# Optimization experiments

Measured on AMD Instinct MI355X. Metric: run time of the kernel, lower is better.

Reference implementation:

```python
import jax, jax.numpy as jnp
import numpy as np
from jax import lax

B, IC, OC, H, W_DIM, K = 8, 64, 64, 256, 512, 3
BLUR_1D = [1.0, 3.0, 3.0, 1.0]
FACTOR = 2
GAIN = 1.0


def _blur_kernel():
    # setup_resample_kernel: outer product of 1D kernel, normalized to sum 1
    k = np.asarray(BLUR_1D, dtype=np.float32)
    k = np.outer(k, k)
    k = k / np.sum(k)
    return k  # [4,4]


def setup_inputs() -> dict:
    key = jax.random.key(0)
    ks = jax.random.split(key, 5)
    x = jax.random.normal(ks[0], (B, IC, H, H), dtype=jnp.float32)
    w = jax.random.normal(ks[1], (B, W_DIM), dtype=jnp.float32)
    # init_std = 1.0 for both weights since lrmul = 1.0
    w_conv = jax.random.normal(ks[2], (K, K, IC, OC), dtype=jnp.float32)
    w_dense = jax.random.normal(ks[3], (W_DIM, IC), dtype=jnp.float32)
    b_mod = jnp.zeros((IC,), dtype=jnp.float32)
    return {"x": x, "w": w, "w_conv": w_conv, "w_dense": w_dense, "b_mod": b_mod}


def reference(x, w, w_conv, w_dense, b_mod):
    k = w_conv.shape[0]
    ic, oc = w_conv.shape[2], w_conv.shape[3]

    # runtime coefs (equalized lr): he_std = gain / sqrt(fan_in), lrmul = 1
    coef_conv = 1.0 / np.sqrt(k * k * ic)
    coef_dense = 1.0 / np.sqrt(w.shape[1])

    # style = Dense(w) + bias (linear act, gain 1) + 1.0   -> [B, IC]
    style = w @ (coef_dense * w_dense) + b_mod + 1.0

    # modulate: [B,k,k,IC,OC]
    wmod = (coef_conv * w_conv)[None] * style[:, None, None, :, None]
    # demodulate over (kh, kw, ic)
    d = lax.rsqrt(jnp.sum(jnp.square(wmod), axis=(1, 2, 3)) + 1e-8)  # [B,OC]
    wmod = wmod * d[:, None, None, None, :]

    # per-sample grouped transposed conv (upsample x2) == lhs-dilated cross-corr
    # with the unflipped modulated weight, padding k-1 on each side.
    w_oihw = jnp.transpose(wmod, (0, 4, 3, 1, 2))  # [B,OC,IC,k,k]

    def up_conv(xb, wb):
        return lax.conv_general_dilated(
            xb[None], wb, window_strides=(1, 1),
            padding=[(k - 1, k - 1), (k - 1, k - 1)],
            lhs_dilation=(FACTOR, FACTOR),
            dimension_numbers=("NCHW", "OIHW", "NCHW"))[0]

    y = jax.vmap(up_conv)(x, w_oihw)  # [B,OC,(H-1)*2+k,(W-1)*2+k] = [B,OC,513,513]

    # upfirdn blur: kernel scaled by gain * factor**2, pad0 = pad1 = 1,
    # true convolution (kernel flipped in reference) applied depthwise.
    kb = jnp.asarray(_blur_kernel() * (GAIN * FACTOR ** 2))  # [4,4]
    fw = kb[::-1, ::-1][None, None]  # [1,1,4,4]
    b_, c_, s1, s2 = y.shape
    y = lax.conv_general_dilated(
        y.reshape(b_ * c_, 1, s1, s2), fw, window_strides=(1, 1),
        padding=[(1, 1), (1, 1)],
        dimension_numbers=("NCHW", "OIHW", "NCHW"))
    # output spatial: s1 + 2 - 4 + 1 = 2H
    return y.reshape(b_, c_, y.shape[2], y.shape[3])
```

## Files before the change

kernel.cpp:

```cpp
#include <hip/hip_runtime.h>

#define NB 8
#define IC 64
#define OC 64
#define HH 256
#define WD 512
#define PP 258

typedef __bf16 bf16x8 __attribute__((ext_vector_type(8)));
typedef float f32x16 __attribute__((ext_vector_type(16)));
typedef float f32x2 __attribute__((ext_vector_type(2)));
typedef unsigned int u32;

__device__ inline void compute_E(const float* __restrict__ w_conv, float stv,
                                 int oc, float E[6][6]) {
  const float coef_conv = 1.0f / 24.0f;
  const float s = stv * coef_conv;
  const int ic = threadIdx.x & 63;

  float wm[3][3];
  float ssq = 0.f;
  #pragma unroll
  for (int kh = 0; kh < 3; ++kh)
    #pragma unroll
    for (int kw = 0; kw < 3; ++kw) {
      float v = w_conv[((kh * 3 + kw) * IC + ic) * OC + oc] * s;
      wm[kh][kw] = v;
      ssq += v * v;
    }
  #pragma unroll
  for (int off = 32; off > 0; off >>= 1) ssq += __shfl_xor(ssq, off);
  const float d = rsqrtf(ssq + 1e-8f);
  #pragma unroll
  for (int kh = 0; kh < 3; ++kh)
    #pragma unroll
    for (int kw = 0; kw < 3; ++kw) wm[kh][kw] *= d;

  const float g[4] = {0.25f, 0.75f, 0.75f, 0.25f};
  #pragma unroll
  for (int a = 0; a < 6; ++a)
    #pragma unroll
    for (int c = 0; c < 6; ++c) {
      float acc = 0.f;
      #pragma unroll
      for (int dh = 0; dh < 3; ++dh) {
        int u = a - dh;
        if (u < 0 || u > 3) continue;
        #pragma unroll
        for (int dw = 0; dw < 3; ++dw) {
          int v = c - dw;
          if (v < 0 || v > 3) continue;
          acc = fmaf(wm[dh][dw], g[u] * g[v], acc);
        }
      }
      E[a][c] = acc;
    }
}

__device__ inline float style_of(const float* __restrict__ w,
                                 const float* __restrict__ w_dense,
                                 const float* __restrict__ b_mod, int b,
                                 int ic) {
  const float coef_dense = 0.044194173824159216f;
  const float* wr = w + b * WD;
  float acc = 0.f;
  for (int k = 0; k < WD; ++k) acc = fmaf(wr[k], w_dense[k * IC + ic], acc);
  return acc * coef_dense + b_mod[ic] + 1.0f;
}

__global__ __launch_bounds__(64) void pwfs_kernel(
    const float* __restrict__ w, const float* __restrict__ w_dense,
    const float* __restrict__ b_mod, const float* __restrict__ w_conv,
    __bf16* __restrict__ PWf) {
  const int oc = blockIdx.x;
  const int b = blockIdx.y;
  const int ic = threadIdx.x;

  float stv = style_of(w, w_dense, b_mod, b, ic);
  float E[6][6];
  compute_E(w_conv, stv, oc, E);

  const int ks = ic >> 4;
  const int h = (ic >> 3) & 1;
  const int e = ic & 7;
  const int lane = (oc & 31) + 32 * h;
  const int ocg = oc >> 5;

  #pragma unroll
  for (int pp = 0; pp < 2; ++pp)
    #pragma unroll
    for (int pq = 0; pq < 2; ++pq) {
      const int ph = pp * 2 + pq;
      #pragma unroll
      for (int j = 0; j < 3; ++j)
        #pragma unroll
        for (int l = 0; l < 3; ++l) {
          const int tap = j * 3 + l;
          float val = E[2 * j + 1 - pp][2 * l + 1 - pq];
          size_t off =
              ((size_t)(((((b * 4 + ph) * 9 + tap) * 2 + ocg) * 4 + ks)) * 64 +
               lane) * 8 + e;
          PWf[off] = (__bf16)val;
        }
    }
}

__global__ __launch_bounds__(256) void xtp_kernel(const float* __restrict__ x,
                                                  __bf16* __restrict__ xTg) {
  __shared__ unsigned short buf[64 * 260];
  const int tid = threadIdx.x;
  const int m = blockIdx.x;
  const int b = blockIdx.y;

  if (m == 256) {
    uint4 z = make_uint4(0, 0, 0, 0);
    for (int i = tid; i < 8224; i += 256) {
      int pix = i >> 3;
      int sub = i & 7;
      int pr, pc;
      if (pix < 258) {
        pr = 0; pc = pix;
      } else if (pix < 516) {
        pr = 257; pc = pix - 258;
      } else {
        int rem = pix - 516;
        pr = 1 + (rem >> 1);
        pc = (rem & 1) ? 257 : 0;
      }
      *(uint4*)(xTg + ((size_t)(b * PP + pr) * PP + pc) * 64 + sub * 8) = z;
    }
    return;
  }

  const int ln = tid & 63, grp = tid >> 6;
  #pragma unroll
  for (int p = 0; p < 16; ++p) {
    const int ic = p * 4 + grp;
    float4 v = *(const float4*)(x + ((size_t)(b * 64 + ic) * 256 + m) * 256 +
                                ln * 4);
    ushort4 u4;
    u4.x = __builtin_bit_cast(unsigned short, (__bf16)v.x);
    u4.y = __builtin_bit_cast(unsigned short, (__bf16)v.y);
    u4.z = __builtin_bit_cast(unsigned short, (__bf16)v.z);
    u4.w = __builtin_bit_cast(unsigned short, (__bf16)v.w);
    *(ushort4*)&buf[ic * 260 + ln * 4] = u4;
  }
  __syncthreads();
  #pragma unroll
  for (int it = 0; it < 8; ++it) {
    int pix = it * 32 + (tid >> 3);
    int g = tid & 7;
    bf16x8 o;
    #pragma unroll
    for (int e = 0; e < 8; ++e)
      o[e] = __builtin_bit_cast(__bf16, buf[(g * 8 + e) * 260 + pix]);
    *(bf16x8*)(xTg + ((size_t)(b * PP + m + 1) * PP + (pix + 1)) * 64 +
               g * 8) = o;
  }
}

#define CMT 16
#define CNT 32
#define XR 18
#define XC 34

__device__ __forceinline__ void loadA(const bf16x8* __restrict__ Av, int phb,
                                      int ocg, int ks, int l, int lane,
                                      bf16x8 A[3][2]) {
  #pragma unroll
  for (int j = 0; j < 3; ++j) {
    const int tap = j * 3 + l;
    #pragma unroll
    for (int pq = 0; pq < 2; ++pq)
      A[j][pq] =
          Av[(size_t)((((phb + pq) * 9 + tap) * 2 + ocg) * 4 + ks) * 64 + lane];
  }
}

#define GLD_LDS(src, dst)                                                \
  __builtin_amdgcn_global_load_lds(                                      \
      (const __attribute__((address_space(1))) void*)(src),              \
      (__attribute__((address_space(3))) void*)(dst), 16, 0, 0)

__device__ __forceinline__ void stage_tile(const __bf16* __restrict__ xTg,
                                           int b, int m0, int n0,
                                           __bf16* xsbuf, int wv, int lane) {
  const int r0 = (18 * wv) >> 3;
  const int r1 = (18 * (wv + 1)) >> 3;
  for (int row = r0; row < r1; ++row) {
    const size_t srow = (size_t)(b * PP + m0 + row) * PP;
    __bf16* ldsrow = xsbuf + row * (XC * 64);
    #pragma unroll
    for (int q = 0; q < 4; ++q) {
      int pix = q * 8 + (lane >> 3);
      int g = (lane & 7) ^ (pix & 7);
      const __bf16* src = xTg + (srow + (n0 + pix)) * 64 + g * 8;
      GLD_LDS(src, ldsrow + q * 512);
    }
    if (lane < 16) {
      int pix = 32 + (lane >> 3);
      int g = (lane & 7) ^ (pix & 7);
      const __bf16* src = xTg + (srow + (n0 + pix)) * 64 + g * 8;
      GLD_LDS(src, ldsrow + 2048);
    }
  }
}

__global__ __launch_bounds__(512, 2) void conv32p_kernel(
    const __bf16* __restrict__ xTg, const __bf16* __restrict__ PWf,
    float* __restrict__ out) {
  __shared__ __bf16 xs[2][XR * XC * 64];

  const int tid = threadIdx.x;
  const int lane = tid & 63;
  const int wv = tid >> 6;
  const int pp = wv & 1;
  const int rh = wv >> 1;

  const int bid = blockIdx.x;
  const int ngrp = bid & 1;
  const int mtile = (bid >> 1) & 15;
  const int ocg = (bid >> 5) & 1;
  const int b = bid >> 6;
  const int m0 = mtile * CMT;

  const int ln31 = lane & 31;
  const int lh = lane >> 5;
  const bf16x8* Av = (const bf16x8*)PWf;
  const int phb = b * 4 + pp * 2;

  stage_tile(xTg, b, m0, ngrp * 128, &xs[0][0], wv, lane);
  asm volatile("s_waitcnt vmcnt(0)" ::: "memory");
  __builtin_amdgcn_s_barrier();

  #pragma unroll 1
  for (int t = 0; t < 4; ++t) {
    const int n0 = ngrp * 128 + t * 32;
    if (t < 3)
      stage_tile(xTg, b, m0, n0 + 32, &xs[(t + 1) & 1][0], wv, lane);

    const __bf16* xb = &xs[t & 1][0];

    f32x16 acc[4][2];
    #pragma unroll
    for (int mw = 0; mw < 4; ++mw)
      #pragma unroll
      for (int pq = 0; pq < 2; ++pq)
        #pragma unroll
        for (int e = 0; e < 16; ++e) acc[mw][pq][e] = 0.f;

    bf16x8 Ac[3][2], An[3][2];
    loadA(Av, phb, ocg, 0, 0, lane, Ac);

    int ks = 0, l = 0;
    #pragma unroll 1
    for (int it = 0; it < 12; ++it) {
      const int ln = (l == 2) ? 0 : l + 1;
      const int ksn = ((l == 2) ? ks + 1 : ks) & 3;
      loadA(Av, phb, ocg, ksn, ln, lane, An);

      bf16x8 Bf[6];
      const int col_t = ln31 + l;
      const int gneed = ks * 2 + lh;
      #pragma unroll
      for (int r = 0; r < 6; ++r) {
        const int lds_row = 4 * rh + r;
        Bf[r] = *(const bf16x8*)(xb + ((lds_row * XC + col_t) * 8 +
                                       (gneed ^ (col_t & 7))) * 8);
      }

      __builtin_amdgcn_s_setprio(1);
      #pragma unroll
      for (int r = 0; r < 6; ++r) {
        #pragma unroll
        for (int j = 0; j < 3; ++j) {
          const int mw = r - j;
          if (mw >= 0 && mw < 4) {
            acc[mw][0] = __builtin_amdgcn_mfma_f32_32x32x16_bf16(
                Ac[j][0], Bf[r], acc[mw][0], 0, 0, 0);
            acc[mw][1] = __builtin_amdgcn_mfma_f32_32x32x16_bf16(
                Ac[j][1], Bf[r], acc[mw][1], 0, 0, 0);
          }
        }
      }
      __builtin_amdgcn_s_setprio(0);

      #pragma unroll
      for (int j = 0; j < 3; ++j)
        #pragma unroll
        for (int pq = 0; pq < 2; ++pq) Ac[j][pq] = An[j][pq];
      ks = ksn;
      l = ln;
    }

    #pragma unroll
    for (int mw = 0; mw < 4; ++mw) {
      const int p = 2 * (m0 + 4 * rh + mw) + pp;
      #pragma unroll
      for (int rr = 0; rr < 16; ++rr) {
        const int oc_loc = (rr & 3) + 8 * (rr >> 2) + 4 * lh;
        const int oc = ocg * 32 + oc_loc;
        size_t off =
            ((size_t)(b * 64 + oc) * 512 + p) * 512 + 2 * n0 + 2 * ln31;
        f32x2 v2;
        v2[0] = acc[mw][0][rr];
        v2[1] = acc[mw][1][rr];
        *(f32x2*)(out + off) = v2;
      }
    }

    asm volatile("s_waitcnt vmcnt(63)" ::: "memory");
    __builtin_amdgcn_s_barrier();
  }
}

__global__ __launch_bounds__(256) void xt_kernel(const float* __restrict__ x,
                                                 __bf16* __restrict__ xT) {
  __shared__ unsigned short buf[64 * 257];
  const int tid = threadIdx.x;
  const int m = blockIdx.x;
  const int b = blockIdx.y;

  for (int ic = 0; ic < 64; ++ic) {
    float v = x[((size_t)(b * 64 + ic) * 256 + m) * 256 + tid];
    buf[ic * 257 + tid] = __builtin_bit_cast(unsigned short, (__bf16)v);
  }
  __syncthreads();
  bf16x8* xTv = (bf16x8*)xT;
  #pragma unroll
  for (int it = 0; it < 8; ++it) {
    int pix = it * 32 + (tid >> 3);
    int g = tid & 7;
    bf16x8 o;
    #pragma unroll
    for (int e = 0; e < 8; ++e)
      o[e] = __builtin_bit_cast(__bf16, buf[(g * 8 + e) * 257 + pix]);
    xTv[((size_t)(b * 256 + m) * 256 + pix) * 8 + g] = o;
  }
}

__global__ __launch_bounds__(512, 2) void conv32_kernel(
    const __bf16* __restrict__ xT, const __bf16* __restrict__ PWf,
    float* __restrict__ out) {
  __shared__ bf16x8 xs[XR * XC * 8];

  const int tid = threadIdx.x;
  const int lane = tid & 63;
  const int w = tid >> 6;
  const int pp = w & 1;
  const int rh = w >> 1;

  const int bx = blockIdx.x;
  const int mtile = bx >> 3;
  const int ntile = bx & 7;
  const int ocg = blockIdx.y;
  const int b = blockIdx.z;
  const int m0 = mtile * CMT;
  const int n0 = ntile * CNT;

  const bf16x8* xTv = (const bf16x8*)xT;
  #pragma unroll
  for (int itr = 0; itr < 10; ++itr) {
    int lin = itr * 512 + tid;
    if (lin < XR * XC * 8) {
      int g = lin & 7;
      int pix = lin >> 3;
      int col = pix % XC;
      int row = pix / XC;
      int gr = m0 - 1 + row;
      int gc = n0 - 1 + col;
      bf16x8 v;
      if ((unsigned)gr < 256u && (unsigned)gc < 256u) {
        v = xTv[((size_t)(b * 256 + gr) * 256 + gc) * 8 + g];
      } else {
        #pragma unroll
        for (int e = 0; e < 8; ++e) v[e] = (__bf16)0.f;
      }
      xs[pix * 8 + (g ^ (col & 7))] = v;
    }
  }
  __syncthreads();

  f32x16 acc[4][2];
  #pragma unroll
  for (int mw = 0; mw < 4; ++mw)
    #pragma unroll
    for (int pq = 0; pq < 2; ++pq)
      #pragma unroll
      for (int e = 0; e < 16; ++e) acc[mw][pq][e] = 0.f;

  const int ln31 = lane & 31;
  const int lh = lane >> 5;
  const bf16x8* Av = (const bf16x8*)PWf;
  const int phb = b * 4 + pp * 2;

  bf16x8 Ac[3][2], An[3][2];
  loadA(Av, phb, ocg, 0, 0, lane, Ac);

  int ks = 0, l = 0;
  #pragma unroll 1
  for (int it = 0; it < 12; ++it) {
    const int ln = (l == 2) ? 0 : l + 1;
    const int ksn = ((l == 2) ? ks + 1 : ks) & 3;
    loadA(Av, phb, ocg, ksn, ln, lane, An);

    bf16x8 Bf[6];
    const int col_t = ln31 + l;
    const int gneed = ks * 2 + lh;
    #pragma unroll
    for (int r = 0; r < 6; ++r) {
      const int lds_row = 4 * rh + r;
      Bf[r] = xs[(lds_row * XC + col_t) * 8 + (gneed ^ (col_t & 7))];
    }

    __builtin_amdgcn_s_setprio(1);
    #pragma unroll
    for (int r = 0; r < 6; ++r) {
      #pragma unroll
      for (int j = 0; j < 3; ++j) {
        const int mw = r - j;
        if (mw >= 0 && mw < 4) {
          acc[mw][0] = __builtin_amdgcn_mfma_f32_32x32x16_bf16(
              Ac[j][0], Bf[r], acc[mw][0], 0, 0, 0);
          acc[mw][1] = __builtin_amdgcn_mfma_f32_32x32x16_bf16(
              Ac[j][1], Bf[r], acc[mw][1], 0, 0, 0);
        }
      }
    }
    __builtin_amdgcn_s_setprio(0);

    #pragma unroll
    for (int j = 0; j < 3; ++j)
      #pragma unroll
      for (int pq = 0; pq < 2; ++pq) Ac[j][pq] = An[j][pq];
    ks = ksn;
    l = ln;
  }

  #pragma unroll
  for (int mw = 0; mw < 4; ++mw) {
    const int p = 2 * (m0 + 4 * rh + mw) + pp;
    #pragma unroll
    for (int rr = 0; rr < 16; ++rr) {
      const int oc_loc = (rr & 3) + 8 * (rr >> 2) + 4 * lh;
      const int oc = ocg * 32 + oc_loc;
      size_t off = ((size_t)(b * 64 + oc) * 512 + p) * 512 + 2 * n0 + 2 * ln31;
      f32x2 v2;
      v2[0] = acc[mw][0][rr];
      v2[1] = acc[mw][1][rr];
      *(f32x2*)(out + off) = v2;
    }
  }
}

__global__ __launch_bounds__(64) void pw_kernel(
    const float* __restrict__ w, const float* __restrict__ w_dense,
    const float* __restrict__ b_mod, const float* __restrict__ w_conv,
    float* __restrict__ PW) {
  const int oc = blockIdx.x;
  const int b = blockIdx.y;
  const int ic = threadIdx.x;
  float stv = style_of(w, w_dense, b_mod, b, ic);
  float E[6][6];
  compute_E(w_conv, stv, oc, E);
  #pragma unroll
  for (int pp = 0; pp < 2; ++pp)
    #pragma unroll
    for (int pq = 0; pq < 2; ++pq)
      #pragma unroll
      for (int j = 0; j < 3; ++j)
        #pragma unroll
        for (int l = 0; l < 3; ++l)
          PW[(((size_t)((b * 4 + pp * 2 + pq) * OC + oc) * IC + ic) * 9) +
             j * 3 + l] = E[2 * j + 1 - pp][2 * l + 1 - pq];
}

#define MT 16
#define NT 64
#define ICC 8
#define XROWS 18
#define XCOLS 66
#define XSTRIDE 68

__global__ __launch_bounds__(256) void conv_kernel(
    const float* __restrict__ x, const float* __restrict__ PW,
    float* __restrict__ out) {
  __shared__ float lds_x[ICC][XROWS][XSTRIDE];
  __shared__ float lds_w[4][ICC][9][4];

  const int tid = threadIdx.x;
  const int tn = tid & 15;
  const int tm = tid >> 4;
  const int bx = blockIdx.x;
  const int ntile = bx & 3;
  const int mtile = bx >> 2;
  const int ocg = blockIdx.y;
  const int b = blockIdx.z;
  const int m0 = mtile * MT;
  const int n0 = ntile * NT;

  float acc[4][4][4];
  #pragma unroll
  for (int o = 0; o < 4; ++o)
    #pragma unroll
    for (int ph = 0; ph < 4; ++ph)
      #pragma unroll
      for (int s = 0; s < 4; ++s) acc[o][ph][s] = 0.f;

  for (int ic0 = 0; ic0 < IC; ic0 += ICC) {
    __syncthreads();
    for (int ici = 0; ici < ICC; ++ici) {
      const float* xsrc = x + (size_t)(b * IC + ic0 + ici) * HH * HH;
      for (int rc = tid; rc < XROWS * XCOLS; rc += 256) {
        int r = rc / XCOLS;
        int c = rc - r * XCOLS;
        int gr = m0 - 1 + r;
        int gc = n0 - 1 + c;
        float v = 0.f;
        if ((unsigned)gr < HH && (unsigned)gc < HH) v = xsrc[gr * HH + gc];
        lds_x[ici][r][c] = v;
      }
    }
    for (int idx = tid; idx < 4 * ICC * 9 * 4; idx += 256) {
      int o = idx / (ICC * 9 * 4);
      int rem = idx - o * (ICC * 9 * 4);
      int ici = rem / 36;
      int r2 = rem - ici * 36;
      int t = r2 >> 2;
      int ph = r2 & 3;
      lds_w[o][ici][t][ph] =
          PW[(((size_t)((b * 4 + ph) * OC + (ocg * 4 + o)) * IC +
               (ic0 + ici)) * 9) + t];
    }
    __syncthreads();
    for (int ici = 0; ici < ICC; ++ici) {
      #pragma unroll
      for (int j = 0; j < 3; ++j) {
        const float* xr = &lds_x[ici][tm + j][tn * 4];
        float4 a4 = *(const float4*)xr;
        float2 a2 = *(const float2*)(xr + 4);
        float xv[6] = {a4.x, a4.y, a4.z, a4.w, a2.x, a2.y};
        #pragma unroll
        for (int l = 0; l < 3; ++l) {
          #pragma unroll
          for (int o = 0; o < 4; ++o) {
            float4 wv = *(const float4*)&lds_w[o][ici][j * 3 + l][0];
            #pragma unroll
            for (int s = 0; s < 4; ++s) {
              acc[o][0][s] = fmaf(wv.x, xv[l + s], acc[o][0][s]);
              acc[o][1][s] = fmaf(wv.y, xv[l + s], acc[o][1][s]);
              acc[o][2][s] = fmaf(wv.z, xv[l + s], acc[o][2][s]);
              acc[o][3][s] = fmaf(wv.w, xv[l + s], acc[o][3][s]);
            }
          }
        }
      }
    }
  }

  #pragma unroll
  for (int o = 0; o < 4; ++o) {
    #pragma unroll
    for (int pp = 0; pp < 2; ++pp) {
      const int p = 2 * (m0 + tm) + pp;
      float* dst = out +
          (((size_t)(b * OC + ocg * 4 + o) * 512 + p) * 512) + 2 * n0 + 8 * tn;
      float4 v0 = make_float4(acc[o][pp * 2 + 0][0], acc[o][pp * 2 + 1][0],
                              acc[o][pp * 2 + 0][1], acc[o][pp * 2 + 1][1]);
      float4 v1 = make_float4(acc[o][pp * 2 + 0][2], acc[o][pp * 2 + 1][2],
                              acc[o][pp * 2 + 0][3], acc[o][pp * 2 + 1][3]);
      *(float4*)dst = v0;
      *(float4*)(dst + 4) = v1;
    }
  }
}

extern "C" void kernel_launch(void* const* d_in, const int* in_sizes, int n_in,
                              void* d_out, int out_size, void* d_ws,
                              size_t ws_size, hipStream_t stream) {
  const float* x = (const float*)d_in[0];
  const float* w = (const float*)d_in[1];
  const float* w_conv = (const float*)d_in[2];
  const float* w_dense = (const float*)d_in[3];
  const float* b_mod = (const float*)d_in[4];
  float* out = (float*)d_out;

  const size_t PWF_BYTES = (size_t)8 * 4 * 9 * 2 * 4 * 64 * 8 * 2;
  const size_t XTG_BYTES = (size_t)8 * PP * PP * 64 * 2;
  const size_t XT_BYTES = (size_t)8 * 256 * 256 * 64 * 2;
  const size_t NEED_NEW = PWF_BYTES + XTG_BYTES;
  const size_t NEED_OLD = PWF_BYTES + XT_BYTES;

  if (ws_size >= NEED_NEW) {
    __bf16* PWf = (__bf16*)d_ws;
    __bf16* xTg = (__bf16*)((char*)d_ws + PWF_BYTES);
    pwfs_kernel<<<dim3(OC, NB), 64, 0, stream>>>(w, w_dense, b_mod, w_conv,
                                                 PWf);
    xtp_kernel<<<dim3(257, NB), 256, 0, stream>>>(x, xTg);
    conv32p_kernel<<<dim3(512), 512, 0, stream>>>(xTg, PWf, out);
  } else if (ws_size >= NEED_OLD) {
    __bf16* PWf = (__bf16*)d_ws;
    __bf16* xT = (__bf16*)((char*)d_ws + PWF_BYTES);
    pwfs_kernel<<<dim3(OC, NB), 64, 0, stream>>>(w, w_dense, b_mod, w_conv,
                                                 PWf);
    xt_kernel<<<dim3(256, NB), 256, 0, stream>>>(x, xT);
    conv32_kernel<<<dim3(128, 2, NB), 512, 0, stream>>>(xT, PWf, out);
  } else {
    float* PW = (float*)d_ws;
    pw_kernel<<<dim3(OC, NB), 64, 0, stream>>>(w, w_dense, b_mod, w_conv, PW);
    conv_kernel<<<dim3(64, 16, NB), 256, 0, stream>>>(x, PW, out);
  }
}
```

Measured before the change: 285.1 us.

## Split conv tile across 16 waves, drop A prefetch, add nontemporal stores

The main conv kernel now runs with 1024 threads per block. Each wave computes 2 output rows instead of 4, using fewer accumulators and B fragments, and the register double-buffering of A weight fragments is removed. Output stores become nontemporal, and the transpose kernel's LDS row stride is widened to change bank mapping. The unused fallback path and its kernels are removed. The intent is higher wave-level parallelism and less register pressure, at the cost of more redundant A loads and LDS reads per output, and no overlap of A loads with MFMA work.

```diff
diff --git a/kernel.cpp b/kernel.cpp
--- a/kernel.cpp
+++ b/kernel.cpp
@@ -10,7 +10,6 @@
 typedef __bf16 bf16x8 __attribute__((ext_vector_type(8)));
 typedef float f32x16 __attribute__((ext_vector_type(16)));
 typedef float f32x2 __attribute__((ext_vector_type(2)));
-typedef unsigned int u32;
 
 __device__ inline void compute_E(const float* __restrict__ w_conv, float stv,
                                  int oc, float E[6][6]) {
@@ -105,9 +104,10 @@
     }
 }
 
+#define XS 268
 __global__ __launch_bounds__(256) void xtp_kernel(const float* __restrict__ x,
                                                   __bf16* __restrict__ xTg) {
-  __shared__ unsigned short buf[64 * 260];
+  __shared__ unsigned short buf[64 * XS];
   const int tid = threadIdx.x;
   const int m = blockIdx.x;
   const int b = blockIdx.y;
@@ -143,7 +143,7 @@
     u4.y = __builtin_bit_cast(unsigned short, (__bf16)v.y);
     u4.z = __builtin_bit_cast(unsigned short, (__bf16)v.z);
     u4.w = __builtin_bit_cast(unsigned short, (__bf16)v.w);
-    *(ushort4*)&buf[ic * 260 + ln * 4] = u4;
+    *(ushort4*)&buf[ic * XS + ln * 4] = u4;
   }
   __syncthreads();
   #pragma unroll
@@ -153,7 +153,7 @@
     bf16x8 o;
     #pragma unroll
     for (int e = 0; e < 8; ++e)
-      o[e] = __builtin_bit_cast(__bf16, buf[(g * 8 + e) * 260 + pix]);
+      o[e] = __builtin_bit_cast(__bf16, buf[(g * 8 + e) * XS + pix]);
     *(bf16x8*)(xTg + ((size_t)(b * PP + m + 1) * PP + (pix + 1)) * 64 +
                g * 8) = o;
   }
@@ -185,8 +185,8 @@
 __device__ __forceinline__ void stage_tile(const __bf16* __restrict__ xTg,
                                            int b, int m0, int n0,
                                            __bf16* xsbuf, int wv, int lane) {
-  const int r0 = (18 * wv) >> 3;
-  const int r1 = (18 * (wv + 1)) >> 3;
+  const int r0 = (18 * wv) >> 4;
+  const int r1 = (18 * (wv + 1)) >> 4;
   for (int row = r0; row < r1; ++row) {
     const size_t srow = (size_t)(b * PP + m0 + row) * PP;
     __bf16* ldsrow = xsbuf + row * (XC * 64);
@@ -206,7 +206,7 @@
   }
 }
 
-__global__ __launch_bounds__(512, 2) void conv32p_kernel(
+__global__ __launch_bounds__(1024) void conv32p_kernel(
     const __bf16* __restrict__ xTg, const __bf16* __restrict__ PWf,
     float* __restrict__ out) {
   __shared__ __bf16 xs[2][XR * XC * 64];
@@ -241,41 +241,37 @@
 
     const __bf16* xb = &xs[t & 1][0];
 
-    f32x16 acc[4][2];
-    #pragma unroll
-    for (int mw = 0; mw < 4; ++mw)
+    f32x16 acc[2][2];
+    #pragma unroll
+    for (int mw = 0; mw < 2; ++mw)
       #pragma unroll
       for (int pq = 0; pq < 2; ++pq)
         #pragma unroll
         for (int e = 0; e < 16; ++e) acc[mw][pq][e] = 0.f;
-
-    bf16x8 Ac[3][2], An[3][2];
-    loadA(Av, phb, ocg, 0, 0, lane, Ac);
 
     int ks = 0, l = 0;
     #pragma unroll 1
     for (int it = 0; it < 12; ++it) {
-      const int ln = (l == 2) ? 0 : l + 1;
-      const int ksn = ((l == 2) ? ks + 1 : ks) & 3;
-      loadA(Av, phb, ocg, ksn, ln, lane, An);
-
-      bf16x8 Bf[6];
+      bf16x8 Ac[3][2];
+      loadA(Av, phb, ocg, ks, l, lane, Ac);
+
+      bf16x8 Bf[4];
       const int col_t = ln31 + l;
       const int gneed = ks * 2 + lh;
       #pragma unroll
-      for (int r = 0; r < 6; ++r) {
-        const int lds_row = 4 * rh + r;
+      for (int r = 0; r < 4; ++r) {
+        const int lds_row = 2 * rh + r;
         Bf[r] = *(const bf16x8*)(xb + ((lds_row * XC + col_t) * 8 +
                                        (gneed ^ (col_t & 7))) * 8);
       }
 
       __builtin_amdgcn_s_setprio(1);
       #pragma unroll
-      for (int r = 0; r < 6; ++r) {
+      for (int r = 0; r < 4; ++r) {
         #pragma unroll
         for (int j = 0; j < 3; ++j) {
           const int mw = r - j;
-          if (mw >= 0 && mw < 4) {
+          if (mw == 0 || mw == 1) {
             acc[mw][0] = __builtin_amdgcn_mfma_f32_32x32x16_bf16(
                 Ac[j][0], Bf[r], acc[mw][0], 0, 0, 0);
             acc[mw][1] = __builtin_amdgcn_mfma_f32_32x32x16_bf16(
@@ -285,17 +281,13 @@
       }
       __builtin_amdgcn_s_setprio(0);
 
-      #pragma unroll
-      for (int j = 0; j < 3; ++j)
-        #pragma unroll
-        for (int pq = 0; pq < 2; ++pq) Ac[j][pq] = An[j][pq];
-      ks = ksn;
-      l = ln;
-    }
-
-    #pragma unroll
-    for (int mw = 0; mw < 4; ++mw) {
-      const int p = 2 * (m0 + 4 * rh + mw) + pp;
+      l = (l == 2) ? 0 : l + 1;
+      ks = (l == 0) ? (ks + 1) & 3 : ks;
+    }
+
+    #pragma unroll
+    for (int mw = 0; mw < 2; ++mw) {
+      const int p = 2 * (m0 + 2 * rh + mw) + pp;
       #pragma unroll
       for (int rr = 0; rr < 16; ++rr) {
         const int oc_loc = (rr & 3) + 8 * (rr >> 2) + 4 * lh;
@@ -305,151 +297,12 @@
         f32x2 v2;
         v2[0] = acc[mw][0][rr];
         v2[1] = acc[mw][1][rr];
-        *(f32x2*)(out + off) = v2;
+        __builtin_nontemporal_store(v2, (f32x2*)(out + off));
       }
     }
 
     asm volatile("s_waitcnt vmcnt(63)" ::: "memory");
     __builtin_amdgcn_s_barrier();
-  }
-}
-
-__global__ __launch_bounds__(256) void xt_kernel(const float* __restrict__ x,
-                                                 __bf16* __restrict__ xT) {
-  __shared__ unsigned short buf[64 * 257];
-  const int tid = threadIdx.x;
-  const int m = blockIdx.x;
-  const int b = blockIdx.y;
-
-  for (int ic = 0; ic < 64; ++ic) {
-    float v = x[((size_t)(b * 64 + ic) * 256 + m) * 256 + tid];
-    buf[ic * 257 + tid] = __builtin_bit_cast(unsigned short, (__bf16)v);
-  }
-  __syncthreads();
-  bf16x8* xTv = (bf16x8*)xT;
-  #pragma unroll
-  for (int it = 0; it < 8; ++it) {
-    int pix = it * 32 + (tid >> 3);
-    int g = tid & 7;
-    bf16x8 o;
-    #pragma unroll
-    for (int e = 0; e < 8; ++e)
-      o[e] = __builtin_bit_cast(__bf16, buf[(g * 8 + e) * 257 + pix]);
-    xTv[((size_t)(b * 256 + m) * 256 + pix) * 8 + g] = o;
-  }
-}
-
-__global__ __launch_bounds__(512, 2) void conv32_kernel(
-    const __bf16* __restrict__ xT, const __bf16* __restrict__ PWf,
-    float* __restrict__ out) {
-  __shared__ bf16x8 xs[XR * XC * 8];
-
-  const int tid = threadIdx.x;
-  const int lane = tid & 63;
-  const int w = tid >> 6;
-  const int pp = w & 1;
-  const int rh = w >> 1;
-
-  const int bx = blockIdx.x;
-  const int mtile = bx >> 3;
-  const int ntile = bx & 7;
-  const int ocg = blockIdx.y;
-  const int b = blockIdx.z;
-  const int m0 = mtile * CMT;
-  const int n0 = ntile * CNT;
-
-  const bf16x8* xTv = (const bf16x8*)xT;
-  #pragma unroll
-  for (int itr = 0; itr < 10; ++itr) {
-    int lin = itr * 512 + tid;
-    if (lin < XR * XC * 8) {
-      int g = lin & 7;
-      int pix = lin >> 3;
-      int col = pix % XC;
-      int row = pix / XC;
-      int gr = m0 - 1 + row;
-      int gc = n0 - 1 + col;
-      bf16x8 v;
-      if ((unsigned)gr < 256u && (unsigned)gc < 256u) {
-        v = xTv[((size_t)(b * 256 + gr) * 256 + gc) * 8 + g];
-      } else {
-        #pragma unroll
-        for (int e = 0; e < 8; ++e) v[e] = (__bf16)0.f;
-      }
-      xs[pix * 8 + (g ^ (col & 7))] = v;
-    }
-  }
-  __syncthreads();
-
-  f32x16 acc[4][2];
-  #pragma unroll
-  for (int mw = 0; mw < 4; ++mw)
-    #pragma unroll
-    for (int pq = 0; pq < 2; ++pq)
-      #pragma unroll
-      for (int e = 0; e < 16; ++e) acc[mw][pq][e] = 0.f;
-
-  const int ln31 = lane & 31;
-  const int lh = lane >> 5;
-  const bf16x8* Av = (const bf16x8*)PWf;
-  const int phb = b * 4 + pp * 2;
-
-  bf16x8 Ac[3][2], An[3][2];
-  loadA(Av, phb, ocg, 0, 0, lane, Ac);
-
-  int ks = 0, l = 0;
-  #pragma unroll 1
-  for (int it = 0; it < 12; ++it) {
-    const int ln = (l == 2) ? 0 : l + 1;
-    const int ksn = ((l == 2) ? ks + 1 : ks) & 3;
-    loadA(Av, phb, ocg, ksn, ln, lane, An);
-
-    bf16x8 Bf[6];
-    const int col_t = ln31 + l;
-    const int gneed = ks * 2 + lh;
-    #pragma unroll
-    for (int r = 0; r < 6; ++r) {
-      const int lds_row = 4 * rh + r;
-      Bf[r] = xs[(lds_row * XC + col_t) * 8 + (gneed ^ (col_t & 7))];
-    }
-
-    __builtin_amdgcn_s_setprio(1);
-    #pragma unroll
-    for (int r = 0; r < 6; ++r) {
-      #pragma unroll
-      for (int j = 0; j < 3; ++j) {
-        const int mw = r - j;
-        if (mw >= 0 && mw < 4) {
-          acc[mw][0] = __builtin_amdgcn_mfma_f32_32x32x16_bf16(
-              Ac[j][0], Bf[r], acc[mw][0], 0, 0, 0);
-          acc[mw][1] = __builtin_amdgcn_mfma_f32_32x32x16_bf16(
-              Ac[j][1], Bf[r], acc[mw][1], 0, 0, 0);
-        }
-      }
-    }
-    __builtin_amdgcn_s_setprio(0);
-
-    #pragma unroll
-    for (int j = 0; j < 3; ++j)
-      #pragma unroll
-      for (int pq = 0; pq < 2; ++pq) Ac[j][pq] = An[j][pq];
-    ks = ksn;
-    l = ln;
-  }
-
-  #pragma unroll
-  for (int mw = 0; mw < 4; ++mw) {
-    const int p = 2 * (m0 + 4 * rh + mw) + pp;
-    #pragma unroll
-    for (int rr = 0; rr < 16; ++rr) {
-      const int oc_loc = (rr & 3) + 8 * (rr >> 2) + 4 * lh;
-      const int oc = ocg * 32 + oc_loc;
-      size_t off = ((size_t)(b * 64 + oc) * 512 + p) * 512 + 2 * n0 + 2 * ln31;
-      f32x2 v2;
-      v2[0] = acc[mw][0][rr];
-      v2[1] = acc[mw][1][rr];
-      *(f32x2*)(out + off) = v2;
-    }
   }
 }
 
@@ -587,9 +440,7 @@
 
   const size_t PWF_BYTES = (size_t)8 * 4 * 9 * 2 * 4 * 64 * 8 * 2;
   const size_t XTG_BYTES = (size_t)8 * PP * PP * 64 * 2;
-  const size_t XT_BYTES = (size_t)8 * 256 * 256 * 64 * 2;
   const size_t NEED_NEW = PWF_BYTES + XTG_BYTES;
-  const size_t NEED_OLD = PWF_BYTES + XT_BYTES;
 
   if (ws_size >= NEED_NEW) {
     __bf16* PWf = (__bf16*)d_ws;
@@ -597,14 +448,7 @@
     pwfs_kernel<<<dim3(OC, NB), 64, 0, stream>>>(w, w_dense, b_mod, w_conv,
                                                  PWf);
     xtp_kernel<<<dim3(257, NB), 256, 0, stream>>>(x, xTg);
-    conv32p_kernel<<<dim3(512), 512, 0, stream>>>(xTg, PWf, out);
-  } else if (ws_size >= NEED_OLD) {
-    __bf16* PWf = (__bf16*)d_ws;
-    __bf16* xT = (__bf16*)((char*)d_ws + PWF_BYTES);
-    pwfs_kernel<<<dim3(OC, NB), 64, 0, stream>>>(w, w_dense, b_mod, w_conv,
-                                                 PWf);
-    xt_kernel<<<dim3(256, NB), 256, 0, stream>>>(x, xT);
-    conv32_kernel<<<dim3(128, 2, NB), 512, 0, stream>>>(xT, PWf, out);
+    conv32p_kernel<<<dim3(512), 1024, 0, stream>>>(xTg, PWf, out);
   } else {
     float* PW = (float*)d_ws;
     pw_kernel<<<dim3(OC, NB), 64, 0, stream>>>(w, w_dense, b_mod, w_conv, PW);
```

New measurement: 278.5 us. -2.3%, faster.
